# Performance work log

Hardware: AMD Instinct MI355X
Metric: run time of the kernel (lower is better)

The kernel has to match this reference:

```python
import jax, jax.numpy as jnp
import numpy as np

N, F, H = 4096, 512, 64
TEMP = 1.0
EPS = 1e-6


def _lin_init(k, fi, fo):
    s = 1.0 / np.sqrt(fi)
    return jax.random.uniform(k, (fi, fo), jnp.float32, -s, s)


def setup_inputs() -> dict:
    key = jax.random.key(0)
    ks = jax.random.split(key, 8)
    adj = jax.random.uniform(ks[0], (N, N), jnp.float32)
    adj = 0.5 * (adj + adj.T)  # symmetric dense adjacency
    x = jax.random.normal(ks[1], (N, F), jnp.float32)
    return {
        'adj': adj,
        'x': x,
        'Wg': _lin_init(ks[2], F, H), 'bg': jnp.zeros((H,), jnp.float32),
        'Wa1': _lin_init(ks[3], H, H), 'ba1': jnp.zeros((H,), jnp.float32),
        'Wa2': _lin_init(ks[4], H, F), 'ba2': jnp.zeros((F,), jnp.float32),
        'Wx1': _lin_init(ks[5], H, H), 'bx1': jnp.zeros((H,), jnp.float32),
        'Wx2': _lin_init(ks[6], H, F), 'bx2': jnp.zeros((F,), jnp.float32),
    }


def _relaxed_bernoulli_st(probs, noise_logistic, temp):
    # pyro RelaxedBernoulliStraightThrough.rsample(): gumbel-sigmoid + hard round w/ ST grad
    p = jnp.clip(probs, EPS, 1.0 - EPS)
    logits = jnp.log(p) - jnp.log1p(-p)
    soft = jax.nn.sigmoid((logits + noise_logistic) / temp)
    hard = jnp.round(soft)
    return soft + jax.lax.stop_gradient(hard - soft)


def _logistic_noise(k, shape):
    u = jax.random.uniform(k, shape, jnp.float32, EPS, 1.0 - EPS)
    return jnp.log(u) - jnp.log1p(-u)


def reference(adj, x, Wg, bg, Wa1, ba1, Wa2, ba2, Wx1, bx1, Wx2, bx2):
    nkey = jax.random.key(42)
    k1, k2 = jax.random.split(nkey)
    # GCN_Body, 1 layer (dropout is eval no-op): h = relu(A @ (X W) + b)
    h = jax.nn.relu(adj @ (x @ Wg) + bg)            # [N, H]
    # MLPA: Z = Linear(ReLU(Linear(h)))
    Z = jax.nn.relu(h @ Wa1 + ba1) @ Wa2 + ba2      # [N, F]
    adj_logits = Z @ Z.T                            # [N, N]
    edge_probs = jax.nn.sigmoid(adj_logits)
    a = _relaxed_bernoulli_st(edge_probs, _logistic_noise(k1, (N, N)), TEMP)
    a = jnp.triu(a, 1)
    a = a + a.T
    # normalize_adj: fill_diagonal_(1); D^{-1/2} A D^{-1/2} (diag matmuls == row/col scaling)
    i = jnp.arange(N)
    a = a.at[i, i].set(1.0)
    d = a.sum(1) ** -0.5                            # [N]
    adj_norm = d[:, None] * a * d[None, :]
    # MLPX feature mask
    mask_logits = jax.nn.relu(h @ Wx1 + bx1) @ Wx2 + bx2  # [N, F]
    mask_probs = jax.nn.sigmoid(mask_logits)
    mask = _relaxed_bernoulli_st(mask_probs, _logistic_noise(k2, (N, F)), TEMP)
    x_new = x * mask
    return (adj_norm, x_new, adj_logits)
```

## Files before the change

### kernel.cpp

```cpp
#include <hip/hip_runtime.h>
#include <cstdint>
#include <cmath>

#define NN 4096
#define FF 512
#define HH 64
#define KSPLIT 8

typedef unsigned short ushort_t;
typedef short bf16x8 __attribute__((ext_vector_type(8)));
typedef float f32x4 __attribute__((ext_vector_type(4)));

__host__ __device__ __forceinline__ uint32_t rotl32(uint32_t x, int r) {
    return (x << r) | (x >> (32 - r));
}

__host__ __device__ __forceinline__ void threefry2x32(uint32_t ks0, uint32_t ks1,
                                                      uint32_t x0, uint32_t x1,
                                                      uint32_t& o0, uint32_t& o1) {
    uint32_t ks2 = ks0 ^ ks1 ^ 0x1BD11BDAu;
    x0 += ks0; x1 += ks1;
    x0 += x1; x1 = rotl32(x1, 13); x1 ^= x0;
    x0 += x1; x1 = rotl32(x1, 15); x1 ^= x0;
    x0 += x1; x1 = rotl32(x1, 26); x1 ^= x0;
    x0 += x1; x1 = rotl32(x1,  6); x1 ^= x0;
    x0 += ks1; x1 += ks2 + 1u;
    x0 += x1; x1 = rotl32(x1, 17); x1 ^= x0;
    x0 += x1; x1 = rotl32(x1, 29); x1 ^= x0;
    x0 += x1; x1 = rotl32(x1, 16); x1 ^= x0;
    x0 += x1; x1 = rotl32(x1, 24); x1 ^= x0;
    x0 += ks2; x1 += ks0 + 2u;
    x0 += x1; x1 = rotl32(x1, 13); x1 ^= x0;
    x0 += x1; x1 = rotl32(x1, 15); x1 ^= x0;
    x0 += x1; x1 = rotl32(x1, 26); x1 ^= x0;
    x0 += x1; x1 = rotl32(x1,  6); x1 ^= x0;
    x0 += ks0; x1 += ks1 + 3u;
    x0 += x1; x1 = rotl32(x1, 17); x1 ^= x0;
    x0 += x1; x1 = rotl32(x1, 29); x1 ^= x0;
    x0 += x1; x1 = rotl32(x1, 16); x1 ^= x0;
    x0 += x1; x1 = rotl32(x1, 24); x1 ^= x0;
    x0 += ks1; x1 += ks2 + 4u;
    x0 += x1; x1 = rotl32(x1, 13); x1 ^= x0;
    x0 += x1; x1 = rotl32(x1, 15); x1 ^= x0;
    x0 += x1; x1 = rotl32(x1, 26); x1 ^= x0;
    x0 += x1; x1 = rotl32(x1,  6); x1 ^= x0;
    x0 += ks2; x1 += ks0 + 5u;
    o0 = x0; o1 = x1;
}

__device__ __forceinline__ uint32_t jax_bits32(uint32_t k0, uint32_t k1, uint32_t j) {
    uint32_t b0, b1;
    threefry2x32(k0, k1, 0u, j, b0, b1);
    return b0 ^ b1;
}

__device__ __forceinline__ float jax_uniform(uint32_t bits) {
    const float minv = 1e-6f;
    const float maxv = (float)(1.0 - 1e-6);
    const float span = maxv - minv;
    float f = __uint_as_float((bits >> 9) | 0x3f800000u) - 1.0f;
    float u = __fadd_rn(__fmul_rn(f, span), minv);
    return fmaxf(minv, u);
}

__device__ __forceinline__ float hard_sample_f(float l, float u) {
    float thr = 1.0f / (1.0f + expf(l));
    return (u > thr) ? 1.0f : 0.0f;
}

__device__ __forceinline__ ushort_t f32_to_bf16_rne(float f) {
    uint32_t x = __float_as_uint(f);
    uint32_t r = (x + 0x7fffu + ((x >> 16) & 1u)) >> 16;
    return (ushort_t)r;
}


__global__ void k_xw(const float* __restrict__ x, const float* __restrict__ Wg,
                     float* __restrict__ T) {
    int col = threadIdx.x;
    int row = blockIdx.x * 4 + threadIdx.y;
    const float* xr = x + row * FF;
    float acc = 0.0f;
    #pragma unroll 4
    for (int k = 0; k < FF; ++k)
        acc += xr[k] * Wg[k * HH + col];
    T[row * HH + col] = acc;
}

__global__ void __launch_bounds__(256)
k_adjT2(const float* __restrict__ adj, const float* __restrict__ T,
        float* __restrict__ partial) {
    __shared__ __align__(16) float As[64][68];
    __shared__ __align__(16) float Ts[64][64];
    int t = threadIdx.x;
    int tx = t & 15, ty = t >> 4;
    int r0 = blockIdx.x * 64;
    int kb = blockIdx.y * (NN / KSPLIT);
    float acc[4][4] = {};
    for (int k0 = 0; k0 < NN / KSPLIT; k0 += 64) {
        __syncthreads();
        for (int n = t; n < 1024; n += 256) {
            int rr = n >> 4, kq = n & 15;
            float4 v = *(const float4*)&adj[(size_t)(r0 + rr) * NN + kb + k0 + kq * 4];
            *(float4*)&As[rr][kq * 4] = v;
        }
        for (int n = t; n < 1024; n += 256) {
            int rr = n >> 4, kq = n & 15;
            float4 v = *(const float4*)&T[(size_t)(kb + k0 + rr) * HH + kq * 4];
            *(float4*)&Ts[rr][kq * 4] = v;
        }
        __syncthreads();
        for (int kk = 0; kk < 64; ++kk) {
            float a[4];
            #pragma unroll
            for (int i = 0; i < 4; ++i) a[i] = As[ty * 4 + i][kk];
            float4 bv = *(float4*)&Ts[kk][tx * 4];
            float b[4] = {bv.x, bv.y, bv.z, bv.w};
            #pragma unroll
            for (int i = 0; i < 4; ++i)
                #pragma unroll
                for (int j = 0; j < 4; ++j)
                    acc[i][j] += a[i] * b[j];
        }
    }
    float* P = partial + (size_t)blockIdx.y * NN * HH;
    #pragma unroll
    for (int i = 0; i < 4; ++i) {
        int row = r0 + ty * 4 + i;
        float4 v = {acc[i][0], acc[i][1], acc[i][2], acc[i][3]};
        *(float4*)&P[(size_t)row * HH + tx * 4] = v;
    }
}

__global__ void k_hred(const float* __restrict__ partial, const float* __restrict__ bg,
                       float* __restrict__ h) {
    int idx = blockIdx.x * 256 + threadIdx.x;
    float s = 0.0f;
    #pragma unroll
    for (int p = 0; p < KSPLIT; ++p) s += partial[(size_t)p * NN * HH + idx];
    float v = s + bg[idx & (HH - 1)];
    h[idx] = v > 0.0f ? v : 0.0f;
}

__global__ void k_small64(const float* __restrict__ A, const float* __restrict__ W,
                          const float* __restrict__ b, float* __restrict__ O) {
    __shared__ float Wl[HH][HH];
    int tx = threadIdx.x, ty = threadIdx.y;
    int tid = ty * 64 + tx;
    for (int n = tid; n < HH * HH; n += 256)
        ((float*)Wl)[n] = W[n];
    __syncthreads();
    int row = blockIdx.x * 4 + ty;
    const float* Ar = A + row * HH;
    float acc = 0.0f;
    #pragma unroll
    for (int k = 0; k < HH; ++k) acc += Ar[k] * Wl[k][tx];
    float v = acc + b[tx];
    O[row * HH + tx] = v > 0.0f ? v : 0.0f;
}

__global__ void k_projZ(const float* __restrict__ A, const float* __restrict__ W,
                        const float* __restrict__ b, ushort_t* __restrict__ Zb) {
    int tx = threadIdx.x, ty = threadIdx.y;
    int row = blockIdx.y * 4 + ty;
    int col = blockIdx.x * 64 + tx;
    const float* Ar = A + row * HH;
    float acc = 0.0f;
    #pragma unroll
    for (int k = 0; k < HH; ++k) acc += Ar[k] * W[k * FF + col];
    Zb[(size_t)row * FF + col] = f32_to_bf16_rne(acc + b[col]);
}

__global__ void k_mask(const float* __restrict__ M1, const float* __restrict__ W,
                       const float* __restrict__ b, const float* __restrict__ x,
                       float* __restrict__ xnew, uint32_t k20, uint32_t k21,
                       float Lmin, float Lmax) {
    int tx = threadIdx.x, ty = threadIdx.y;
    int row = blockIdx.y * 4 + ty;
    int col = blockIdx.x * 64 + tx;
    const float* Ar = M1 + row * HH;
    float acc = 0.0f;
    #pragma unroll
    for (int k = 0; k < HH; ++k) acc += Ar[k] * W[k * FF + col];
    float ml = acc + b[col];
    float l = ml < Lmin ? Lmin : (ml > Lmax ? Lmax : ml);
    uint32_t idx = (uint32_t)row * FF + (uint32_t)col;
    float u = jax_uniform(jax_bits32(k20, k21, idx));
    float m = hard_sample_f(l, u);
    xnew[idx] = (m != 0.0f) ? x[idx] : 0.0f;
}

__global__ void __launch_bounds__(256)
k_zzt(const ushort_t* __restrict__ Zb, float* __restrict__ out2,
      uint32_t* __restrict__ mask, float* __restrict__ rowsum,
      uint32_t k10, uint32_t k11, float Lmin, float Lmax) {
    __shared__ __align__(16) ushort_t At[128][72];
    __shared__ __align__(16) ushort_t Bt[128][72];
    __shared__ int rs_i[128];
    int t = threadIdx.x;
    int lane = t & 63, w = t >> 6;
    int lr = lane & 15, lk = lane >> 4;
    if (t < 128) rs_i[t] = 0;
    int b = blockIdx.x;
    int bi = b >> 5, bj = b & 31;
    int rbase = bi * 128, cbase = bj * 128;
    f32x4 acc[2][8] = {};
    for (int k0 = 0; k0 < FF; k0 += 64) {
        __syncthreads();
        for (int n = t; n < 1024; n += 256) {
            int rr = n >> 3, ck = n & 7;
            *(uint4*)&At[rr][ck * 8] = *(const uint4*)&Zb[(size_t)(rbase + rr) * FF + k0 + ck * 8];
            *(uint4*)&Bt[rr][ck * 8] = *(const uint4*)&Zb[(size_t)(cbase + rr) * FF + k0 + ck * 8];
        }
        __syncthreads();
        #pragma unroll
        for (int ks = 0; ks < 2; ++ks) {
            bf16x8 a0 = *(const bf16x8*)&At[w * 32 + lr][ks * 32 + lk * 8];
            bf16x8 a1 = *(const bf16x8*)&At[w * 32 + 16 + lr][ks * 32 + lk * 8];
            #pragma unroll
            for (int j = 0; j < 8; ++j) {
                bf16x8 bb = *(const bf16x8*)&Bt[j * 16 + lr][ks * 32 + lk * 8];
                acc[0][j] = __builtin_amdgcn_mfma_f32_16x16x32_bf16(a0, bb, acc[0][j], 0, 0, 0);
                acc[1][j] = __builtin_amdgcn_mfma_f32_16x16x32_bf16(a1, bb, acc[1][j], 0, 0, 0);
            }
        }
    }
    #pragma unroll
    for (int it = 0; it < 2; ++it) {
        #pragma unroll
        for (int reg = 0; reg < 4; ++reg) {
            unsigned long long ball[8];
            int rg = rbase + w * 32 + it * 16 + lk * 4 + reg;
            #pragma unroll
            for (int j = 0; j < 8; ++j) {
                float z = acc[it][j][reg];
                int cg = cbase + j * 16 + lr;
                out2[(size_t)rg * NN + cg] = z;
                float l = z < Lmin ? Lmin : (z > Lmax ? Lmax : z);
                int lo = rg < cg ? rg : cg;
                int hi = rg < cg ? cg : rg;
                uint32_t idx = (uint32_t)lo * NN + (uint32_t)hi;
                float u = jax_uniform(jax_bits32(k10, k11, idx));
                float thr = 1.0f / (1.0f + expf(l));
                int bit = (rg == cg) ? 1 : (u > thr ? 1 : 0);
                ball[j] = __ballot(bit);
            }
            if (lane < 16) {
                int lkp = lane >> 2, wi = lane & 3;
                unsigned long long bl = (wi & 2) ? ((wi & 1) ? ball[6] : ball[4])
                                                 : ((wi & 1) ? ball[2] : ball[0]);
                unsigned long long bh = (wi & 2) ? ((wi & 1) ? ball[7] : ball[5])
                                                 : ((wi & 1) ? ball[3] : ball[1]);
                uint32_t lo16 = (uint32_t)(bl >> (lkp * 16)) & 0xffffu;
                uint32_t hi16 = (uint32_t)(bh >> (lkp * 16)) & 0xffffu;
                uint32_t wv = lo16 | (hi16 << 16);
                int rl = w * 32 + it * 16 + lkp * 4 + reg;
                mask[(size_t)(rbase + rl) * (NN / 32) + (cbase >> 5) + wi] = wv;
                atomicAdd(&rs_i[rl], (int)__popc(wv));
            }
        }
    }
    __syncthreads();
    if (t < 128)
        atomicAdd(&rowsum[rbase + t], (float)rs_i[t]);
}

__global__ void k_deg(const float* __restrict__ rowsum, float* __restrict__ dvec) {
    int i = blockIdx.x * 256 + threadIdx.x;
    dvec[i] = 1.0f / sqrtf(rowsum[i]);
}

__global__ void k_scale2(const uint32_t* __restrict__ mask,
                         const float* __restrict__ dvec, float* __restrict__ out0) {
    size_t idx = ((size_t)blockIdx.x * 256 + threadIdx.x) * 4;
    int r = (int)(idx >> 12);
    int c = (int)(idx & 4095);
    uint32_t wv = mask[idx >> 5];
    int sh = (int)(idx & 31);
    float dr = dvec[r];
    float4 dc = *(const float4*)&dvec[c];
    float4 o;
    o.x = ((wv >> (sh + 0)) & 1u) ? dr * dc.x : 0.0f;
    o.y = ((wv >> (sh + 1)) & 1u) ? dr * dc.y : 0.0f;
    o.z = ((wv >> (sh + 2)) & 1u) ? dr * dc.z : 0.0f;
    o.w = ((wv >> (sh + 3)) & 1u) ? dr * dc.w : 0.0f;
    *(float4*)&out0[idx] = o;
}

extern "C" void kernel_launch(void* const* d_in, const int* in_sizes, int n_in,
                              void* d_out, int out_size, void* d_ws, size_t ws_size,
                              hipStream_t stream) {
    const float* adj = (const float*)d_in[0];
    const float* x   = (const float*)d_in[1];
    const float* Wg  = (const float*)d_in[2];
    const float* bg  = (const float*)d_in[3];
    const float* Wa1 = (const float*)d_in[4];
    const float* ba1 = (const float*)d_in[5];
    const float* Wa2 = (const float*)d_in[6];
    const float* ba2 = (const float*)d_in[7];
    const float* Wx1 = (const float*)d_in[8];
    const float* bx1 = (const float*)d_in[9];
    const float* Wx2 = (const float*)d_in[10];
    const float* bx2 = (const float*)d_in[11];

    float* out0 = (float*)d_out;
    float* out1 = out0 + (size_t)NN * NN;
    float* out2 = out1 + (size_t)NN * FF;

    float* T       = (float*)d_ws;
    float* h       = T + NN * HH;
    float* A1      = h + NN * HH;
    float* M1      = A1 + NN * HH;
    ushort_t* Zb   = (ushort_t*)(M1 + NN * HH);
    float* partial = (float*)(Zb + (size_t)NN * FF);
    float* dvec    = partial + (size_t)KSPLIT * NN * HH;
    float* rowsum  = dvec + NN;
    uint32_t* mask = (uint32_t*)partial;

    uint32_t k1a, k1b, k2a, k2b;
    threefry2x32(0u, 42u, 0u, 0u, k1a, k1b);
    threefry2x32(0u, 42u, 0u, 1u, k2a, k2b);

    const float Lmax = (float)(std::log(1.0 - 1e-6) - std::log1p(-(1.0 - 1e-6)));
    const float Lmin = (float)(std::log(1e-6) - std::log1p(-1e-6));

    k_xw<<<NN / 4, dim3(64, 4), 0, stream>>>(x, Wg, T);
    k_adjT2<<<dim3(64, KSPLIT), 256, 0, stream>>>(adj, T, partial);
    k_hred<<<NN * HH / 256, 256, 0, stream>>>(partial, bg, h);
    k_small64<<<NN / 4, dim3(64, 4), 0, stream>>>(h, Wa1, ba1, A1);
    k_projZ<<<dim3(FF / 64, NN / 4), dim3(64, 4), 0, stream>>>(A1, Wa2, ba2, Zb);

    hipMemsetAsync(rowsum, 0, NN * sizeof(float), stream);
    k_zzt<<<1024, 256, 0, stream>>>(Zb, out2, mask, rowsum, k1a, k1b, Lmin, Lmax);
    k_deg<<<NN / 256, 256, 0, stream>>>(rowsum, dvec);
    k_scale2<<<NN * NN / 4 / 256, 256, 0, stream>>>(mask, dvec, out0);

    k_small64<<<NN / 4, dim3(64, 4), 0, stream>>>(h, Wx1, bx1, M1);
    k_mask<<<dim3(FF / 64, NN / 4), dim3(64, 4), 0, stream>>>(M1, Wx2, bx2, x, out1,
                                                              k2a, k2b, Lmin, Lmax);
}
```

Baseline: 466.2 us.

## Split ZZ^T GEMM from Bernoulli sampling into separate kernels

The fused ZZ^T GEMM plus edge-sampling kernel is split in two. The GEMM kernel now only writes the logits. A new sampling kernel rereads the logits, builds the packed mask bits per 32-column word, and reduces row sums with wave shuffles. This removes the ballot shuffling and heavy RNG work from the MFMA kernel's epilogue, which may lower register pressure and help the GEMM's occupancy. The cost is an extra full 64MB read of the logits matrix and one more kernel launch.

```diff
diff --git a/kernel.cpp b/kernel.cpp
--- a/kernel.cpp
+++ b/kernel.cpp
@@ -191,16 +191,12 @@
 }
 
 __global__ void __launch_bounds__(256)
-k_zzt(const ushort_t* __restrict__ Zb, float* __restrict__ out2,
-      uint32_t* __restrict__ mask, float* __restrict__ rowsum,
-      uint32_t k10, uint32_t k11, float Lmin, float Lmax) {
+k_zzt_gemm(const ushort_t* __restrict__ Zb, float* __restrict__ out2) {
     __shared__ __align__(16) ushort_t At[128][72];
     __shared__ __align__(16) ushort_t Bt[128][72];
-    __shared__ int rs_i[128];
     int t = threadIdx.x;
     int lane = t & 63, w = t >> 6;
     int lr = lane & 15, lk = lane >> 4;
-    if (t < 128) rs_i[t] = 0;
     int b = blockIdx.x;
     int bi = b >> 5, bj = b & 31;
     int rbase = bi * 128, cbase = bj * 128;
@@ -227,42 +223,50 @@
     }
     #pragma unroll
     for (int it = 0; it < 2; ++it) {
+        int rg = rbase + w * 32 + it * 16 + lk * 4;
         #pragma unroll
         for (int reg = 0; reg < 4; ++reg) {
-            unsigned long long ball[8];
-            int rg = rbase + w * 32 + it * 16 + lk * 4 + reg;
             #pragma unroll
             for (int j = 0; j < 8; ++j) {
-                float z = acc[it][j][reg];
-                int cg = cbase + j * 16 + lr;
-                out2[(size_t)rg * NN + cg] = z;
-                float l = z < Lmin ? Lmin : (z > Lmax ? Lmax : z);
-                int lo = rg < cg ? rg : cg;
-                int hi = rg < cg ? cg : rg;
-                uint32_t idx = (uint32_t)lo * NN + (uint32_t)hi;
-                float u = jax_uniform(jax_bits32(k10, k11, idx));
-                float thr = 1.0f / (1.0f + expf(l));
-                int bit = (rg == cg) ? 1 : (u > thr ? 1 : 0);
-                ball[j] = __ballot(bit);
+                out2[(size_t)(rg + reg) * NN + cbase + j * 16 + lr] = acc[it][j][reg];
             }
-            if (lane < 16) {
-                int lkp = lane >> 2, wi = lane & 3;
-                unsigned long long bl = (wi & 2) ? ((wi & 1) ? ball[6] : ball[4])
-                                                 : ((wi & 1) ? ball[2] : ball[0]);
-                unsigned long long bh = (wi & 2) ? ((wi & 1) ? ball[7] : ball[5])
-                                                 : ((wi & 1) ? ball[3] : ball[1]);
-                uint32_t lo16 = (uint32_t)(bl >> (lkp * 16)) & 0xffffu;
-                uint32_t hi16 = (uint32_t)(bh >> (lkp * 16)) & 0xffffu;
-                uint32_t wv = lo16 | (hi16 << 16);
-                int rl = w * 32 + it * 16 + lkp * 4 + reg;
-                mask[(size_t)(rbase + rl) * (NN / 32) + (cbase >> 5) + wi] = wv;
-                atomicAdd(&rs_i[rl], (int)__popc(wv));
-            }
-        }
-    }
-    __syncthreads();
-    if (t < 128)
-        atomicAdd(&rowsum[rbase + t], (float)rs_i[t]);
+        }
+    }
+}
+
+__global__ void __launch_bounds__(256)
+k_sample(const float* __restrict__ out2, uint32_t* __restrict__ mask,
+         float* __restrict__ rowsum, uint32_t k10, uint32_t k11,
+         float Lmin, float Lmax) {
+    int g = blockIdx.x * 256 + threadIdx.x;
+    int r = g >> 7;
+    int wd = g & 127;
+    const float* zr = out2 + (size_t)r * NN + wd * 32;
+    uint32_t word = 0;
+    #pragma unroll
+    for (int q = 0; q < 8; ++q) {
+        float4 zv = *(const float4*)&zr[q * 4];
+        float za[4] = {zv.x, zv.y, zv.z, zv.w};
+        #pragma unroll
+        for (int e4 = 0; e4 < 4; ++e4) {
+            int e = q * 4 + e4;
+            int c = wd * 32 + e;
+            float z = za[e4];
+            float l = z < Lmin ? Lmin : (z > Lmax ? Lmax : z);
+            int lo = r < c ? r : c;
+            int hi = r < c ? c : r;
+            uint32_t idx = (uint32_t)lo * NN + (uint32_t)hi;
+            float u = jax_uniform(jax_bits32(k10, k11, idx));
+            float thr = 1.0f / (1.0f + expf(l));
+            uint32_t bit = (r == c) ? 1u : (u > thr ? 1u : 0u);
+            word |= bit << e;
+        }
+    }
+    mask[g] = word;
+    int pc = __popc(word);
+    #pragma unroll
+    for (int off = 32; off; off >>= 1) pc += __shfl_down(pc, off);
+    if ((threadIdx.x & 63) == 0) atomicAdd(&rowsum[r], (float)pc);
 }
 
 __global__ void k_deg(const float* __restrict__ rowsum, float* __restrict__ dvec) {
@@ -330,8 +334,11 @@
     k_small64<<<NN / 4, dim3(64, 4), 0, stream>>>(h, Wa1, ba1, A1);
     k_projZ<<<dim3(FF / 64, NN / 4), dim3(64, 4), 0, stream>>>(A1, Wa2, ba2, Zb);
 
+    k_zzt_gemm<<<1024, 256, 0, stream>>>(Zb, out2);
+
     hipMemsetAsync(rowsum, 0, NN * sizeof(float), stream);
-    k_zzt<<<1024, 256, 0, stream>>>(Zb, out2, mask, rowsum, k1a, k1b, Lmin, Lmax);
+    k_sample<<<NN * NN / 32 / 256, 256, 0, stream>>>(out2, mask, rowsum,
+                                                     k1a, k1b, Lmin, Lmax);
     k_deg<<<NN / 256, 256, 0, stream>>>(rowsum, dvec);
     k_scale2<<<NN * NN / 4 / 256, 256, 0, stream>>>(mask, dvec, out0);
 
```

Result: no change. 462.6 us (-0.8%).
